# Kernel tuning notes

Measured on AMD Instinct MI355X. Metric: run time of the kernel, lower is better.

The kernel has to match this reference:

```python
import jax, jax.numpy as jnp
import numpy as np

DIM = 1024
NUM_HEADS = 16
HEAD_DIM = DIM // NUM_HEADS
SCALE = HEAD_DIM ** -0.5


def setup_inputs() -> dict:
    key = jax.random.key(0)
    k1, k2, k3 = jax.random.split(key, 3)
    B, N = 4, 2048
    x = jax.random.normal(k1, (B, N, DIM), dtype=jnp.float32)
    w_qkv = jax.random.normal(k2, (DIM, 3 * DIM), dtype=jnp.float32) * (DIM ** -0.5)
    w_proj = jax.random.normal(k3, (DIM, DIM), dtype=jnp.float32) * (DIM ** -0.5)
    b_proj = jnp.zeros((DIM,), dtype=jnp.float32)
    return {"x": x, "w_qkv": w_qkv, "w_proj": w_proj, "b_proj": b_proj}


def reference(x, w_qkv, w_proj, b_proj):
    B, N, C = x.shape
    H, D = NUM_HEADS, HEAD_DIM
    # qkv projection: (B,N,3C) -> (3,B,H,N,D)
    qkv = (x @ w_qkv).reshape(B, N, 3, H, D).transpose(2, 0, 3, 1, 4)
    q, k, v = qkv[0], qkv[1], qkv[2]
    # full attention scores (B,H,N,N), scaled
    attn = jnp.einsum("bhnd,bhmd->bhnm", q, k) * SCALE
    attn = jax.nn.softmax(attn, axis=-1)
    out = jnp.einsum("bhnm,bhmd->bhnd", attn, v)
    out = out.transpose(0, 2, 1, 3).reshape(B, N, C)
    return out @ w_proj + b_proj
```

## Files before the change

### kernel.cpp

```cpp
#include <hip/hip_runtime.h>
#include <stdint.h>

#define DIM 1024
#define NHEADS 16
#define HDIM 64
#define BATCH 4
#define SEQ 2048
#define NTOK (BATCH*SEQ)
#define SCALE_L2E 0.1803368801111244f

typedef float f32x4 __attribute__((ext_vector_type(4)));
typedef short s16x8 __attribute__((ext_vector_type(8)));

#define MFMA16(a,b,c) __builtin_amdgcn_mfma_f32_16x16x32_bf16((a),(b),(c),0,0,0)

static __device__ __forceinline__ uint16_t f2bf(float f) {
    uint32_t u = __builtin_bit_cast(uint32_t, f);
    return (uint16_t)((u + 0x7FFFu + ((u >> 16) & 1u)) >> 16);
}

static __device__ __forceinline__ float bf2f(uint16_t u) {
    uint32_t v = ((uint32_t)u) << 16;
    return __builtin_bit_cast(float, v);
}

static __device__ __forceinline__ uint32_t cvt_pk_bf16(float lo, float hi) {
    uint32_t r;
    asm("v_cvt_pk_bf16_f32 %0, %1, %2" : "=v"(r) : "v"(lo), "v"(hi));
    return r;
}

static __device__ __forceinline__ void gl_lds16(const void* g, void* l) {
    __builtin_amdgcn_global_load_lds(
        (const __attribute__((address_space(1))) unsigned int*)g,
        (__attribute__((address_space(3))) unsigned int*)l, 16, 0, 0);
}

__global__ void convert_f32_bf16(const float* __restrict__ in, uint16_t* __restrict__ out) {
    const int i = blockIdx.x * blockDim.x + threadIdx.x;
    const float4 a = ((const float4*)in)[2*i];
    const float4 b = ((const float4*)in)[2*i + 1];
    ushort4 lo, hi;
    lo.x = f2bf(a.x); lo.y = f2bf(a.y); lo.z = f2bf(a.z); lo.w = f2bf(a.w);
    hi.x = f2bf(b.x); hi.y = f2bf(b.y); hi.z = f2bf(b.z); hi.w = f2bf(b.w);
    ((ushort4*)out)[2*i]     = lo;
    ((ushort4*)out)[2*i + 1] = hi;
}

__global__ void transpose_conv(const float* __restrict__ w, uint16_t* __restrict__ wT,
                               int K, int N) {
    __shared__ float t[32][33];
    const int tx = threadIdx.x, ty = threadIdx.y;
    const int n0 = blockIdx.x * 32, k0 = blockIdx.y * 32;
    #pragma unroll
    for (int i = 0; i < 4; ++i)
        t[ty + i*8][tx] = w[(size_t)(k0 + ty + i*8) * N + n0 + tx];
    __syncthreads();
    #pragma unroll
    for (int i = 0; i < 4; ++i)
        wT[(size_t)(n0 + ty + i*8) * K + k0 + tx] = f2bf(t[tx][ty + i*8]);
}

template <int MODE>
__global__ __launch_bounds__(256) void gemm_bt(
    const uint16_t* __restrict__ A, const uint16_t* __restrict__ B,
    void* __restrict__ C, const float* __restrict__ bias,
    int M, int N, int K)
{
    __shared__ uint16_t As[128*64];
    __shared__ uint16_t Bs[128*64];
    const int tid  = threadIdx.x;
    const int lane = tid & 63;
    const int wid  = tid >> 6;
    const int wm = wid >> 1, wn = wid & 1;
    const long row0 = (long)blockIdx.y * 128;
    const long col0 = (long)blockIdx.x * 128;

    const int sr  = lane >> 3;
    const int scb = (lane & 7) * 16;

    f32x4 acc[4][4] = {};

    for (int kt = 0; kt < K; kt += 64) {
        #pragma unroll
        for (int j = 0; j < 4; ++j) {
            const int r = (wid*4 + j)*8 + sr;
            const int c = (scb ^ ((r & 7) << 4)) >> 1;
            gl_lds16(&A[(row0 + r)*K + kt + c], &As[(wid*4 + j)*512]);
            gl_lds16(&B[(col0 + r)*K + kt + c], &Bs[(wid*4 + j)*512]);
        }
        __syncthreads();
        #pragma unroll
        for (int ks = 0; ks < 2; ++ks) {
            const int xb = (ks*32 + (lane >> 4)*8) * 2;
            s16x8 av[4], bv[4];
            #pragma unroll
            for (int f = 0; f < 4; ++f) {
                const int ra = wm*64 + f*16 + (lane & 15);
                av[f] = *(const s16x8*)((const char*)As + ra*128 + (xb ^ ((ra & 7) << 4)));
                const int rb = wn*64 + f*16 + (lane & 15);
                bv[f] = *(const s16x8*)((const char*)Bs + rb*128 + (xb ^ ((rb & 7) << 4)));
            }
            #pragma unroll
            for (int i = 0; i < 4; ++i)
                #pragma unroll
                for (int j = 0; j < 4; ++j)
                    acc[i][j] = MFMA16(av[i], bv[j], acc[i][j]);
        }
        __syncthreads();
    }

    #pragma unroll
    for (int i = 0; i < 4; ++i) {
        const long row = row0 + wm*64 + i*16 + (lane >> 4)*4;
        #pragma unroll
        for (int j = 0; j < 4; ++j) {
            const long col = col0 + wn*64 + j*16 + (lane & 15);
            #pragma unroll
            for (int r = 0; r < 4; ++r) {
                if (MODE == 0)
                    ((uint16_t*)C)[(row + r)*N + col] = f2bf(acc[i][j][r]);
                else
                    ((float*)C)[(row + r)*N + col] = acc[i][j][r] + bias[col];
            }
        }
    }
}

__global__ void rearrange_qk(const uint16_t* __restrict__ qkv,
                             uint16_t* __restrict__ Qb, uint16_t* __restrict__ Kb) {
    const int i = blockIdx.x * blockDim.x + threadIdx.x;
    const int s  = i >> 20;
    const int r  = i & 1048575;
    const int d8 = r & 7;
    const int n  = (r >> 3) & 2047;
    const int bh = r >> 14;
    const int b = bh >> 4, h = bh & 15;
    uint4 v = *(const uint4*)&qkv[((size_t)(b*SEQ + n))*3*DIM + s*DIM + h*HDIM + d8*8];
    if (s == 0) {
        union { uint4 v4; uint16_t u[8]; } t;
        t.v4 = v;
        #pragma unroll
        for (int e = 0; e < 8; ++e) t.u[e] = f2bf(bf2f(t.u[e]) * SCALE_L2E);
        v = t.v4;
    }
    uint16_t* dst = s ? Kb : Qb;
    *(uint4*)&dst[((size_t)bh*SEQ + n)*HDIM + d8*8] = v;
}

__global__ void transpose_v(const uint16_t* __restrict__ qkv, uint16_t* __restrict__ VT) {
    __shared__ uint16_t t[64][72];
    const int nt = blockIdx.x;
    const int bh = blockIdx.y;
    const int b = bh >> 4, h = bh & 15;
    const int tid = threadIdx.x;
    #pragma unroll
    for (int j = 0; j < 2; ++j) {
        const int idx = tid + j*256;
        const int n_l = idx >> 3, c = (idx & 7)*8;
        const uint4 v = *(const uint4*)&qkv[((size_t)(b*SEQ + nt*64 + n_l))*3*DIM + 2*DIM + h*HDIM + c];
        *(uint4*)&t[n_l][c] = v;
    }
    __syncthreads();
    #pragma unroll
    for (int j = 0; j < 2; ++j) {
        const int idx = tid + j*256;
        const int d = idx >> 3, n0 = (idx & 7)*8;
        union { uint16_t u[8]; uint4 v; } tmp;
        #pragma unroll
        for (int e = 0; e < 8; ++e) tmp.u[e] = t[n0 + e][d];
        *(uint4*)&VT[((size_t)bh*HDIM + d)*SEQ + nt*64 + n0] = tmp.v;
    }
}

__global__ __launch_bounds__(256) void attn_kernel(
    const uint16_t* __restrict__ Q, const uint16_t* __restrict__ Kg,
    const uint16_t* __restrict__ VT, uint16_t* __restrict__ O)
{
    __shared__ uint16_t Ks[64*64];
    __shared__ uint16_t Vs[64*64];
    __shared__ uint16_t Ps[128*64];
    const int tid = threadIdx.x, lane = tid & 63, wid = tid >> 6;
    const int qt = blockIdx.x, bh = blockIdx.y;
    const int b = bh >> 4, h = bh & 15;
    const uint16_t* Qh = Q  + (size_t)bh * SEQ * HDIM;
    const uint16_t* Kh = Kg + (size_t)bh * SEQ * HDIM;
    const uint16_t* Vh = VT + (size_t)bh * HDIM * SEQ;
    const int qbase = qt*128 + wid*32;
    const int g = lane >> 4, q15 = lane & 15;
    const int swl = (lane & 7) << 4;

    s16x8 bq[2][2];
    #pragma unroll
    for (int i = 0; i < 2; ++i)
        #pragma unroll
        for (int ks = 0; ks < 2; ++ks)
            bq[i][ks] = *(const s16x8*)&Qh[(size_t)(qbase + i*16 + q15)*HDIM + ks*32 + g*8];

    f32x4 o[2][4] = {};
    f32x4 lacc[2] = {};

    const int sr  = lane >> 3;
    const int scb = (lane & 7) * 16;

    for (int it = 0; it < 32; ++it) {
        #pragma unroll
        for (int j = 0; j < 2; ++j) {
            const int r = (wid*2 + j)*8 + sr;
            const int c = (scb ^ ((r & 7) << 4)) >> 1;
            gl_lds16(&Kh[(size_t)(it*64 + r)*HDIM + c], &Ks[(wid*2 + j)*512]);
            gl_lds16(&Vh[(size_t)r*SEQ + it*64 + c],    &Vs[(wid*2 + j)*512]);
        }
        __syncthreads();

        f32x4 st[2][4] = {};
        #pragma unroll
        for (int ks = 0; ks < 2; ++ks) {
            const int xb = (ks*32 + g*8) * 2;
            s16x8 ak[4];
            #pragma unroll
            for (int f = 0; f < 4; ++f) {
                const int rk = f*16 + q15;
                ak[f] = *(const s16x8*)((const char*)Ks + rk*128 + (xb ^ ((rk & 7) << 4)));
            }
            #pragma unroll
            for (int i = 0; i < 2; ++i)
                #pragma unroll
                for (int f = 0; f < 4; ++f)
                    st[i][f] = MFMA16(ak[f], bq[i][ks], st[i][f]);
        }

        #pragma unroll
        for (int i = 0; i < 2; ++i) {
            #pragma unroll
            for (int f = 0; f < 4; ++f) {
                #pragma unroll
                for (int r = 0; r < 4; ++r)
                    st[i][f][r] = __builtin_amdgcn_exp2f(st[i][f][r]);
            }
            lacc[i] += (st[i][0] + st[i][1]) + (st[i][2] + st[i][3]);
        }

        #pragma unroll
        for (int i = 0; i < 2; ++i) {
            char* base = (char*)Ps + (wid*32 + i*16 + q15)*128;
            #pragma unroll
            for (int f = 0; f < 4; ++f) {
                uint2 w;
                w.x = cvt_pk_bf16(st[i][f][0], st[i][f][1]);
                w.y = cvt_pk_bf16(st[i][f][2], st[i][f][3]);
                *(uint2*)(base + ((f*32 + g*8) ^ swl)) = w;
            }
        }

        #pragma unroll
        for (int ks = 0; ks < 2; ++ks) {
            s16x8 pa[2], vb[4];
            #pragma unroll
            for (int i = 0; i < 2; ++i)
                pa[i] = *(const s16x8*)((const char*)Ps + (wid*32 + i*16 + q15)*128
                                         + ((ks*64 + g*16) ^ swl));
            const int xbv = (ks*32 + g*8) * 2;
            #pragma unroll
            for (int f = 0; f < 4; ++f) {
                const int rv = f*16 + q15;
                vb[f] = *(const s16x8*)((const char*)Vs + rv*128 + (xbv ^ ((rv & 7) << 4)));
            }
            #pragma unroll
            for (int i = 0; i < 2; ++i)
                #pragma unroll
                for (int f = 0; f < 4; ++f)
                    o[i][f] = MFMA16(pa[i], vb[f], o[i][f]);
        }
        __syncthreads();
    }

    #pragma unroll
    for (int i = 0; i < 2; ++i) {
        float ls = (lacc[i][0] + lacc[i][1]) + (lacc[i][2] + lacc[i][3]);
        ls += __shfl_xor(ls, 16);
        ls += __shfl_xor(ls, 32);
        #pragma unroll
        for (int r = 0; r < 4; ++r) {
            const float l_r = __shfl(ls, g*4 + r);
            const float inv = 1.0f / l_r;
            const int n = qbase + i*16 + g*4 + r;
            const size_t base = ((size_t)b*SEQ + n)*DIM + h*HDIM;
            #pragma unroll
            for (int f = 0; f < 4; ++f)
                O[base + f*16 + q15] = f2bf(o[i][f][r] * inv);
        }
    }
}

extern "C" void kernel_launch(void* const* d_in, const int* in_sizes, int n_in,
                              void* d_out, int out_size, void* d_ws, size_t ws_size,
                              hipStream_t stream)
{
    const float* x      = (const float*)d_in[0];
    const float* w_qkv  = (const float*)d_in[1];
    const float* w_proj = (const float*)d_in[2];
    const float* b_proj = (const float*)d_in[3];
    float* out = (float*)d_out;

    uint16_t* xb     = (uint16_t*)d_ws;
    uint16_t* wqkvT  = xb     + (size_t)NTOK*DIM;
    uint16_t* wprojT = wqkvT  + (size_t)3*DIM*DIM;
    uint16_t* qkv    = wprojT + (size_t)DIM*DIM;
    uint16_t* Qb     = qkv    + (size_t)NTOK*3*DIM;
    uint16_t* Kb     = Qb     + (size_t)NTOK*DIM;
    uint16_t* VTb    = Kb     + (size_t)NTOK*DIM;
    uint16_t* attn_o = qkv;

    convert_f32_bf16<<<dim3(NTOK*DIM/8/256), dim3(256), 0, stream>>>(x, xb);
    transpose_conv<<<dim3(96, 32), dim3(32, 8), 0, stream>>>(w_qkv, wqkvT, DIM, 3*DIM);
    transpose_conv<<<dim3(32, 32), dim3(32, 8), 0, stream>>>(w_proj, wprojT, DIM, DIM);
    gemm_bt<0><<<dim3(24, 64), dim3(256), 0, stream>>>(xb, wqkvT, qkv, nullptr, NTOK, 3*DIM, DIM);
    rearrange_qk<<<dim3(8192), dim3(256), 0, stream>>>(qkv, Qb, Kb);
    transpose_v<<<dim3(32, 64), dim3(256), 0, stream>>>(qkv, VTb);
    attn_kernel<<<dim3(16, 64), dim3(256), 0, stream>>>(Qb, Kb, VTb, attn_o);
    gemm_bt<1><<<dim3(8, 64), dim3(256), 0, stream>>>(attn_o, wprojT, out, b_proj, NTOK, DIM, DIM);
}
```

Before: 219.4 us.

## Fuse QK head layout into projection GEMM, compute V transposed directly, double-buffer attention

The QKV projection is split in two. A new GEMM writes Q (pre-scaled) and K straight into per-head layout. V is produced already transposed by computing W_v^T·x^T with the existing GEMM. This removes the rearrange and transpose kernels along with their extra global-memory round trip. The attention kernel also double-buffers its K/V shared tiles so the next tile's loads overlap compute, at the cost of more LDS and possibly lower occupancy. The new GEMM's epilogue does scattered 2-byte stores.

```diff
diff --git a/kernel.cpp b/kernel.cpp
--- a/kernel.cpp
+++ b/kernel.cpp
@@ -17,11 +17,6 @@
 static __device__ __forceinline__ uint16_t f2bf(float f) {
     uint32_t u = __builtin_bit_cast(uint32_t, f);
     return (uint16_t)((u + 0x7FFFu + ((u >> 16) & 1u)) >> 16);
-}
-
-static __device__ __forceinline__ float bf2f(uint16_t u) {
-    uint32_t v = ((uint32_t)u) << 16;
-    return __builtin_bit_cast(float, v);
 }
 
 static __device__ __forceinline__ uint32_t cvt_pk_bf16(float lo, float hi) {
@@ -127,49 +122,70 @@
     }
 }
 
-__global__ void rearrange_qk(const uint16_t* __restrict__ qkv,
-                             uint16_t* __restrict__ Qb, uint16_t* __restrict__ Kb) {
-    const int i = blockIdx.x * blockDim.x + threadIdx.x;
-    const int s  = i >> 20;
-    const int r  = i & 1048575;
-    const int d8 = r & 7;
-    const int n  = (r >> 3) & 2047;
-    const int bh = r >> 14;
-    const int b = bh >> 4, h = bh & 15;
-    uint4 v = *(const uint4*)&qkv[((size_t)(b*SEQ + n))*3*DIM + s*DIM + h*HDIM + d8*8];
-    if (s == 0) {
-        union { uint4 v4; uint16_t u[8]; } t;
-        t.v4 = v;
-        #pragma unroll
-        for (int e = 0; e < 8; ++e) t.u[e] = f2bf(bf2f(t.u[e]) * SCALE_L2E);
-        v = t.v4;
-    }
-    uint16_t* dst = s ? Kb : Qb;
-    *(uint4*)&dst[((size_t)bh*SEQ + n)*HDIM + d8*8] = v;
-}
-
-__global__ void transpose_v(const uint16_t* __restrict__ qkv, uint16_t* __restrict__ VT) {
-    __shared__ uint16_t t[64][72];
-    const int nt = blockIdx.x;
-    const int bh = blockIdx.y;
-    const int b = bh >> 4, h = bh & 15;
-    const int tid = threadIdx.x;
-    #pragma unroll
-    for (int j = 0; j < 2; ++j) {
-        const int idx = tid + j*256;
-        const int n_l = idx >> 3, c = (idx & 7)*8;
-        const uint4 v = *(const uint4*)&qkv[((size_t)(b*SEQ + nt*64 + n_l))*3*DIM + 2*DIM + h*HDIM + c];
-        *(uint4*)&t[n_l][c] = v;
-    }
-    __syncthreads();
-    #pragma unroll
-    for (int j = 0; j < 2; ++j) {
-        const int idx = tid + j*256;
-        const int d = idx >> 3, n0 = (idx & 7)*8;
-        union { uint16_t u[8]; uint4 v; } tmp;
-        #pragma unroll
-        for (int e = 0; e < 8; ++e) tmp.u[e] = t[n0 + e][d];
-        *(uint4*)&VT[((size_t)bh*HDIM + d)*SEQ + nt*64 + n0] = tmp.v;
+__global__ __launch_bounds__(256) void gemm_qk(
+    const uint16_t* __restrict__ A, const uint16_t* __restrict__ B,
+    uint16_t* __restrict__ Qb, uint16_t* __restrict__ Kb)
+{
+    __shared__ uint16_t As[128*64];
+    __shared__ uint16_t Bs[128*64];
+    const int K = DIM;
+    const int tid  = threadIdx.x;
+    const int lane = tid & 63;
+    const int wid  = tid >> 6;
+    const int wm = wid >> 1, wn = wid & 1;
+    const long row0 = (long)blockIdx.y * 128;
+    const long col0 = (long)blockIdx.x * 128;
+
+    const int sr  = lane >> 3;
+    const int scb = (lane & 7) * 16;
+
+    f32x4 acc[4][4] = {};
+
+    for (int kt = 0; kt < K; kt += 64) {
+        #pragma unroll
+        for (int j = 0; j < 4; ++j) {
+            const int r = (wid*4 + j)*8 + sr;
+            const int c = (scb ^ ((r & 7) << 4)) >> 1;
+            gl_lds16(&A[(row0 + r)*K + kt + c], &As[(wid*4 + j)*512]);
+            gl_lds16(&B[(col0 + r)*K + kt + c], &Bs[(wid*4 + j)*512]);
+        }
+        __syncthreads();
+        #pragma unroll
+        for (int ks = 0; ks < 2; ++ks) {
+            const int xb = (ks*32 + (lane >> 4)*8) * 2;
+            s16x8 av[4], bv[4];
+            #pragma unroll
+            for (int f = 0; f < 4; ++f) {
+                const int ra = wm*64 + f*16 + (lane & 15);
+                av[f] = *(const s16x8*)((const char*)As + ra*128 + (xb ^ ((ra & 7) << 4)));
+                const int rb = wn*64 + f*16 + (lane & 15);
+                bv[f] = *(const s16x8*)((const char*)Bs + rb*128 + (xb ^ ((rb & 7) << 4)));
+            }
+            #pragma unroll
+            for (int i = 0; i < 4; ++i)
+                #pragma unroll
+                for (int j = 0; j < 4; ++j)
+                    acc[i][j] = MFMA16(av[i], bv[j], acc[i][j]);
+        }
+        __syncthreads();
+    }
+
+    #pragma unroll
+    for (int i = 0; i < 4; ++i) {
+        const int rowl = wm*64 + i*16 + (lane >> 4)*4;
+        #pragma unroll
+        for (int j = 0; j < 4; ++j) {
+            const int col = (int)col0 + wn*64 + j*16 + (lane & 15);
+            const int s = col >> 10, h = (col >> 6) & 15, d = col & 63;
+            uint16_t* dst = s ? Kb : Qb;
+            const float sc = s ? 1.0f : SCALE_L2E;
+            #pragma unroll
+            for (int r = 0; r < 4; ++r) {
+                const long rr = row0 + rowl + r;
+                const int b = (int)(rr >> 11), n = (int)(rr & 2047);
+                dst[((size_t)(b*NHEADS + h)*SEQ + n)*HDIM + d] = f2bf(acc[i][j][r] * sc);
+            }
+        }
     }
 }
 
@@ -177,15 +193,15 @@
     const uint16_t* __restrict__ Q, const uint16_t* __restrict__ Kg,
     const uint16_t* __restrict__ VT, uint16_t* __restrict__ O)
 {
-    __shared__ uint16_t Ks[64*64];
-    __shared__ uint16_t Vs[64*64];
+    __shared__ uint16_t Ks[2][64*64];
+    __shared__ uint16_t Vs[2][64*64];
     __shared__ uint16_t Ps[128*64];
     const int tid = threadIdx.x, lane = tid & 63, wid = tid >> 6;
     const int qt = blockIdx.x, bh = blockIdx.y;
     const int b = bh >> 4, h = bh & 15;
     const uint16_t* Qh = Q  + (size_t)bh * SEQ * HDIM;
     const uint16_t* Kh = Kg + (size_t)bh * SEQ * HDIM;
-    const uint16_t* Vh = VT + (size_t)bh * HDIM * SEQ;
+    const uint16_t* Vh = VT + (size_t)h * HDIM * NTOK + (size_t)b * SEQ;
     const int qbase = qt*128 + wid*32;
     const int g = lane >> 4, q15 = lane & 15;
     const int swl = (lane & 7) << 4;
@@ -202,16 +218,25 @@
 
     const int sr  = lane >> 3;
     const int scb = (lane & 7) * 16;
+    const int stg_c = (scb ^ ((sr) << 4)) >> 1;
+
+    #define STAGE(bf, t)                                                          \
+        _Pragma("unroll")                                                         \
+        for (int j = 0; j < 2; ++j) {                                             \
+            const int r = (wid*2 + j)*8 + sr;                                     \
+            gl_lds16(&Kh[(size_t)((t)*64 + r)*HDIM + stg_c], &Ks[bf][(wid*2 + j)*512]); \
+            gl_lds16(&Vh[(size_t)r*NTOK + (t)*64 + stg_c],   &Vs[bf][(wid*2 + j)*512]); \
+        }
+
+    STAGE(0, 0)
+    __syncthreads();
 
     for (int it = 0; it < 32; ++it) {
-        #pragma unroll
-        for (int j = 0; j < 2; ++j) {
-            const int r = (wid*2 + j)*8 + sr;
-            const int c = (scb ^ ((r & 7) << 4)) >> 1;
-            gl_lds16(&Kh[(size_t)(it*64 + r)*HDIM + c], &Ks[(wid*2 + j)*512]);
-            gl_lds16(&Vh[(size_t)r*SEQ + it*64 + c],    &Vs[(wid*2 + j)*512]);
-        }
-        __syncthreads();
+        const int cur = it & 1;
+        if (it < 31) STAGE(cur ^ 1, it + 1)
+
+        const uint16_t* ksb = Ks[cur];
+        const uint16_t* vsb = Vs[cur];
 
         f32x4 st[2][4] = {};
         #pragma unroll
@@ -221,7 +246,7 @@
             #pragma unroll
             for (int f = 0; f < 4; ++f) {
                 const int rk = f*16 + q15;
-                ak[f] = *(const s16x8*)((const char*)Ks + rk*128 + (xb ^ ((rk & 7) << 4)));
+                ak[f] = *(const s16x8*)((const char*)ksb + rk*128 + (xb ^ ((rk & 7) << 4)));
             }
             #pragma unroll
             for (int i = 0; i < 2; ++i)
@@ -264,7 +289,7 @@
             #pragma unroll
             for (int f = 0; f < 4; ++f) {
                 const int rv = f*16 + q15;
-                vb[f] = *(const s16x8*)((const char*)Vs + rv*128 + (xbv ^ ((rv & 7) << 4)));
+                vb[f] = *(const s16x8*)((const char*)vsb + rv*128 + (xbv ^ ((rv & 7) << 4)));
             }
             #pragma unroll
             for (int i = 0; i < 2; ++i)
@@ -272,8 +297,10 @@
                 for (int f = 0; f < 4; ++f)
                     o[i][f] = MFMA16(pa[i], vb[f], o[i][f]);
         }
-        __syncthreads();
-    }
+
+        __syncthreads();
+    }
+    #undef STAGE
 
     #pragma unroll
     for (int i = 0; i < 2; ++i) {
@@ -306,18 +333,17 @@
     uint16_t* xb     = (uint16_t*)d_ws;
     uint16_t* wqkvT  = xb     + (size_t)NTOK*DIM;
     uint16_t* wprojT = wqkvT  + (size_t)3*DIM*DIM;
-    uint16_t* qkv    = wprojT + (size_t)DIM*DIM;
-    uint16_t* Qb     = qkv    + (size_t)NTOK*3*DIM;
+    uint16_t* Qb     = wprojT + (size_t)DIM*DIM;
     uint16_t* Kb     = Qb     + (size_t)NTOK*DIM;
     uint16_t* VTb    = Kb     + (size_t)NTOK*DIM;
-    uint16_t* attn_o = qkv;
+    uint16_t* attn_o = VTb    + (size_t)NTOK*DIM;
 
     convert_f32_bf16<<<dim3(NTOK*DIM/8/256), dim3(256), 0, stream>>>(x, xb);
     transpose_conv<<<dim3(96, 32), dim3(32, 8), 0, stream>>>(w_qkv, wqkvT, DIM, 3*DIM);
     transpose_conv<<<dim3(32, 32), dim3(32, 8), 0, stream>>>(w_proj, wprojT, DIM, DIM);
-    gemm_bt<0><<<dim3(24, 64), dim3(256), 0, stream>>>(xb, wqkvT, qkv, nullptr, NTOK, 3*DIM, DIM);
-    rearrange_qk<<<dim3(8192), dim3(256), 0, stream>>>(qkv, Qb, Kb);
-    transpose_v<<<dim3(32, 64), dim3(256), 0, stream>>>(qkv, VTb);
+    gemm_qk<<<dim3(16, 64), dim3(256), 0, stream>>>(xb, wqkvT, Qb, Kb);
+    gemm_bt<0><<<dim3(64, 8), dim3(256), 0, stream>>>(wqkvT + (size_t)2*DIM*DIM, xb,
+                                                      VTb, nullptr, DIM, NTOK, DIM);
     attn_kernel<<<dim3(16, 64), dim3(256), 0, stream>>>(Qb, Kb, VTb, attn_o);
     gemm_bt<1><<<dim3(8, 64), dim3(256), 0, stream>>>(attn_o, wprojT, out, b_proj, NTOK, DIM, DIM);
 }
```

Result: faster. 209.1 us (-4.7%).
